# Kernel optimization log

Hardware: AMD Instinct MI355X
Metric: run time of the kernel (lower is better)

Reference implementation:

```python
import jax, jax.numpy as jnp
import numpy as np

V_DIM, Q_DIM, NUM_HID = 2048, 1024, 1024
B, K, N = 64, 12, 36


def setup_inputs() -> dict:
    key = jax.random.key(0)
    ks = jax.random.split(key, 8)
    v = jax.random.normal(ks[0], (B, K, N, V_DIM), dtype=jnp.float32)
    q = jax.random.normal(ks[1], (B, K, Q_DIM), dtype=jnp.float32)
    # FCNet layer: weight_norm(Linear(v_dim+q_dim, num_hid), dim=None) + ReLU
    W1 = jax.random.normal(ks[2], (NUM_HID, V_DIM + Q_DIM), dtype=jnp.float32) * 0.02
    g1 = jnp.asarray(1.0, dtype=jnp.float32)  # weight_norm gain (scalar, dim=None)
    b1 = jnp.zeros((NUM_HID,), dtype=jnp.float32)
    # final: weight_norm(Linear(num_hid, 1), dim=None)
    W2 = jax.random.normal(ks[3], (1, NUM_HID), dtype=jnp.float32) * 0.02
    g2 = jnp.asarray(1.0, dtype=jnp.float32)
    b2 = jnp.zeros((1,), dtype=jnp.float32)
    return {"v": v, "q": q, "W1": W1, "g1": g1, "b1": b1, "W2": W2, "g2": g2, "b2": b2}


def reference(v, q, W1, g1, b1, W2, g2, b2):
    # weight_norm with dim=None: W_eff = g * W / ||W||_F (g is a scalar)
    W1e = g1 * W1 / jnp.linalg.norm(W1)   # [num_hid, v_dim+q_dim]
    W2e = g2 * W2 / jnp.linalg.norm(W2)   # [1, num_hid]
    # Avoid materializing the repeated+concatenated [B,K,N,v_dim+q_dim] tensor:
    # cat(v, broadcast(q)) @ W1e^T == v @ W1v^T + q @ W1q^T (q term broadcast over N)
    W1v = W1e[:, :V_DIM]                  # [num_hid, v_dim]
    W1q = W1e[:, V_DIM:]                  # [num_hid, q_dim]
    hv = jnp.einsum('bknv,hv->bknh', v, W1v)          # [B,K,N,num_hid]
    hq = jnp.einsum('bkq,hq->bkh', q, W1q)            # [B,K,num_hid]
    joint = jax.nn.relu(hv + hq[:, :, None, :] + b1)  # FCNet: weight-norm Linear + ReLU
    logits = jnp.einsum('bknh,oh->bkno', joint, W2e) + b2  # [B,K,N,1]
    w = jax.nn.softmax(logits, axis=1)                # softmax over k (dim 1)
    return w
```

## Files before the change

### kernel.cpp

```cpp
#include <hip/hip_runtime.h>

#define V_DIM   2048
#define Q_DIM   1024
#define NUM_HID 1024
#define BB 64
#define KK 12
#define NN 36
#define M_ROWS (BB*KK*NN)
#define BKROWS (BB*KK)

typedef unsigned short u16;
typedef __bf16 bf16x8  __attribute__((ext_vector_type(8)));
typedef u16    ushort8 __attribute__((ext_vector_type(8)));
typedef float  floatx4 __attribute__((ext_vector_type(4)));

__device__ __forceinline__ unsigned cvtpk(float lo, float hi) {
    unsigned r;
    asm("v_cvt_pk_bf16_f32 %0, %1, %2" : "=v"(r) : "v"(lo), "v"(hi));
    return r;
}

__device__ __forceinline__ void gload16(const u16* g, u16* l) {
    __builtin_amdgcn_global_load_lds((const __attribute__((address_space(1))) void*)g,
                                     (__attribute__((address_space(3))) void*)l, 16, 0, 0);
}

__global__ void convert_w1_kernel(const float* __restrict__ W1,
                                  u16* __restrict__ W1v, u16* __restrict__ W1q,
                                  const float* __restrict__ W2,
                                  const float* __restrict__ g1,
                                  const float* __restrict__ g2,
                                  float* __restrict__ wsf)
{
    int s = blockIdx.x * 256 + threadIdx.x;
    int h = s / 384, g = s % 384;
    const float4* p = (const float4*)(W1 + (size_t)h * (V_DIM + Q_DIM) + g * 8);
    float4 a = p[0], b = p[1];
    float ss = a.x*a.x + a.y*a.y + a.z*a.z + a.w*a.w
             + b.x*b.x + b.y*b.y + b.z*b.z + b.w*b.w;
    unsigned d0 = cvtpk(a.x, a.y), d1 = cvtpk(a.z, a.w);
    unsigned d2 = cvtpk(b.x, b.y), d3 = cvtpk(b.z, b.w);
    uint4 o = make_uint4(d0, d1, d2, d3);
    if (g < 256) *(uint4*)(W1v + (size_t)h * V_DIM + g * 8) = o;
    else         *(uint4*)(W1q + (size_t)h * Q_DIM + (g - 256) * 8) = o;
    #pragma unroll
    for (int off = 32; off > 0; off >>= 1) ss += __shfl_down(ss, off);
    __shared__ float red[4];
    __shared__ bool  last;
    if ((threadIdx.x & 63) == 0) red[threadIdx.x >> 6] = ss;
    __syncthreads();
    if (threadIdx.x == 0) {
        atomicAdd(wsf, red[0] + red[1] + red[2] + red[3]);
        __threadfence();
        unsigned t = atomicAdd((unsigned*)(wsf + 1), 1u);
        last = (t == gridDim.x - 1);
    }
    __syncthreads();
    if (last) {
        float4 w = ((const float4*)W2)[threadIdx.x];
        float s2 = w.x*w.x + w.y*w.y + w.z*w.z + w.w*w.w;
        #pragma unroll
        for (int off = 32; off > 0; off >>= 1) s2 += __shfl_down(s2, off);
        __shared__ float red2[4];
        if ((threadIdx.x & 63) == 0) red2[threadIdx.x >> 6] = s2;
        __syncthreads();
        if (threadIdx.x == 0) {
            float w2ss = red2[0] + red2[1] + red2[2] + red2[3];
            float w1ss = atomicAdd(wsf, 0.0f);
            wsf[2] = g1[0] / sqrtf(w1ss);
            wsf[3] = g2[0] / sqrtf(w2ss);
        }
    }
}

template<int GK, bool MAIN>
__global__ __launch_bounds__(256, 2)
void gemm_kernel(const float* __restrict__ Asrc,
                 const u16*   __restrict__ Bsrc,
                 float*       __restrict__ outp,
                 const float* __restrict__ hq,
                 const float* __restrict__ b1,
                 const float* __restrict__ W2,
                 const float* __restrict__ scl)
{
    __shared__ u16 As[128 * 64];
    __shared__ u16 Bs[128 * 64];

    const int tid  = threadIdx.x;
    const int lane = tid & 63;
    const int wv   = tid >> 6;
    const int wm   = wv & 1;
    const int wn   = wv >> 1;
    const int quad = lane >> 4;
    const int l15  = lane & 15;

    const int bid  = blockIdx.y * 8 + blockIdx.x;
    const int nwg  = gridDim.x * gridDim.y;
    const int tile = (bid & 7) * (nwg >> 3) + (bid >> 3);
    const int tx   = tile & 7;
    const int ty   = tile >> 3;
    const int m0   = ty * 128;
    const int n0   = tx * 128;

    floatx4 acc[4][4];
    #pragma unroll
    for (int i = 0; i < 4; i++)
        #pragma unroll
        for (int j = 0; j < 4; j++)
            acc[i][j] = (floatx4){0.f, 0.f, 0.f, 0.f};

    for (int kt = 0; kt < GK / 64; ++kt) {
        const int k0 = kt * 64;
        __syncthreads();
        #pragma unroll
        for (int it = 0; it < 4; ++it) {
            int s = tid + 256 * it;
            int r = s >> 3, g = s & 7;
            const float4* gp = (const float4*)(Asrc + (size_t)(m0 + r) * GK + k0 + g * 8);
            float4 f0 = gp[0];
            float4 f1 = gp[1];
            unsigned d0 = cvtpk(f0.x, f0.y), d1 = cvtpk(f0.z, f0.w);
            unsigned d2 = cvtpk(f1.x, f1.y), d3 = cvtpk(f1.z, f1.w);
            *(uint4*)(&As[r * 64 + ((g ^ (r & 7)) * 8)]) = make_uint4(d0, d1, d2, d3);
        }
        #pragma unroll
        for (int it = 0; it < 4; ++it) {
            int sbase = it * 256 + wv * 64;
            int s = sbase + lane;
            int c = s >> 3, g = s & 7;
            int gs = g ^ (c & 7);
            gload16(Bsrc + (size_t)(n0 + c) * GK + k0 + gs * 8, &Bs[sbase * 8]);
        }
        __syncthreads();
        #pragma unroll
        for (int ks = 0; ks < 2; ++ks) {
            bf16x8 af[4], bfr[4];
            #pragma unroll
            for (int i = 0; i < 4; i++) {
                int rA = wm * 64 + i * 16 + l15;
                int offA = (ks * 32 + quad * 8) ^ ((rA & 7) << 3);
                af[i] = *(const bf16x8*)(&As[rA * 64 + offA]);
            }
            #pragma unroll
            for (int j = 0; j < 4; j++) {
                int c = wn * 64 + j * 16 + l15;
                int offB = (ks * 32 + quad * 8) ^ ((c & 7) << 3);
                bfr[j] = *(const bf16x8*)(&Bs[c * 64 + offB]);
            }
            #pragma unroll
            for (int i = 0; i < 4; i++)
                #pragma unroll
                for (int j = 0; j < 4; j++)
                    acc[i][j] = __builtin_amdgcn_mfma_f32_16x16x32_bf16(af[i], bfr[j], acc[i][j], 0, 0, 0);
        }
    }

    if constexpr (MAIN) {
        const float s1 = scl[2];
        int   cg[4];
        float w2v[4], b1v[4];
        #pragma unroll
        for (int j = 0; j < 4; j++) {
            cg[j]  = n0 + wn * 64 + j * 16 + l15;
            w2v[j] = W2[cg[j]];
            b1v[j] = b1[cg[j]];
        }
        #pragma unroll
        for (int i = 0; i < 4; i++) {
            #pragma unroll
            for (int r = 0; r < 4; r++) {
                const int mg = m0 + wm * 64 + i * 16 + quad * 4 + r;
                const int bk = mg / NN;
                float p = 0.f;
                #pragma unroll
                for (int j = 0; j < 4; j++) {
                    float pre = s1 * (acc[i][j][r] + hq[(size_t)bk * NUM_HID + cg[j]]) + b1v[j];
                    p += fmaxf(pre, 0.f) * w2v[j];
                }
                p += __shfl_xor(p, 1);
                p += __shfl_xor(p, 2);
                p += __shfl_xor(p, 4);
                p += __shfl_xor(p, 8);
                if (l15 == 0)
                    outp[(size_t)mg * 16 + tx * 2 + wn] = p;
            }
        }
    } else {
        #pragma unroll
        for (int i = 0; i < 4; i++)
            #pragma unroll
            for (int r = 0; r < 4; r++) {
                const int mg = m0 + wm * 64 + i * 16 + quad * 4 + r;
                #pragma unroll
                for (int j = 0; j < 4; j++) {
                    const int c = n0 + wn * 64 + j * 16 + l15;
                    outp[(size_t)mg * NUM_HID + c] = acc[i][j][r];
                }
            }
    }
}

__global__ void softmax_kernel(const float* __restrict__ part,
                               const float* __restrict__ scl,
                               const float* __restrict__ b2,
                               float* __restrict__ out)
{
    int t = blockIdx.x * 64 + threadIdx.x;
    int b = t / NN, n = t % NN;
    float s2 = scl[3], bias = b2[0];
    float lg[KK];
    float mx = -1e30f;
    #pragma unroll
    for (int k = 0; k < KK; k++) {
        int m = (b * KK + k) * NN + n;
        const float4* pp = (const float4*)(part + (size_t)m * 16);
        float4 a0 = pp[0], a1 = pp[1], a2 = pp[2], a3 = pp[3];
        float s = (a0.x + a0.y + a0.z + a0.w) + (a1.x + a1.y + a1.z + a1.w)
                + (a2.x + a2.y + a2.z + a2.w) + (a3.x + a3.y + a3.z + a3.w);
        lg[k] = s2 * s + bias;
        mx = fmaxf(mx, lg[k]);
    }
    float den = 0.f;
    #pragma unroll
    for (int k = 0; k < KK; k++) { lg[k] = expf(lg[k] - mx); den += lg[k]; }
    float inv = 1.0f / den;
    #pragma unroll
    for (int k = 0; k < KK; k++) out[(size_t)((b * KK + k) * NN + n)] = lg[k] * inv;
}

extern "C" void kernel_launch(void* const* d_in, const int* in_sizes, int n_in,
                              void* d_out, int out_size, void* d_ws, size_t ws_size,
                              hipStream_t stream)
{
    (void)in_sizes; (void)n_in; (void)out_size; (void)ws_size;
    const float* v  = (const float*)d_in[0];
    const float* q  = (const float*)d_in[1];
    const float* W1 = (const float*)d_in[2];
    const float* g1 = (const float*)d_in[3];
    const float* b1 = (const float*)d_in[4];
    const float* W2 = (const float*)d_in[5];
    const float* g2 = (const float*)d_in[6];
    const float* b2 = (const float*)d_in[7];
    float* out = (float*)d_out;

    char*  ws   = (char*)d_ws;
    float* wsf  = (float*)ws;
    float* hq   = (float*)(ws + 16);
    u16*   W1v  = (u16*)  (ws + 16 + 3145728);
    u16*   W1q  = (u16*)  (ws + 16 + 3145728 + 4194304);
    float* part = (float*)(ws + 16 + 3145728 + 4194304 + 2097152);

    hipMemsetAsync(d_ws, 0, 16, stream);
    convert_w1_kernel<<<1536, 256, 0, stream>>>(W1, W1v, W1q, W2, g1, g2, wsf);
    gemm_kernel<Q_DIM, false><<<dim3(8, 6), 256, 0, stream>>>(
        q, W1q, hq, nullptr, nullptr, nullptr, wsf);
    gemm_kernel<V_DIM, true><<<dim3(8, 216), 256, 0, stream>>>(
        v, W1v, part, hq, b1, W2, wsf);
    softmax_kernel<<<36, 64, 0, stream>>>(part, wsf, b2, out);
}
```

Baseline: 545.2 us.

## Double-buffer LDS tiles and prefetch A registers two stages ahead in GEMM

Replaces the single-buffered K-loop with a ping-pong LDS scheme. The B tile for the next step is loaded straight to LDS, and the fp32 A tile is prefetched into registers two iterations ahead, then converted to bf16 and written into the alternate buffer while the current tile feeds MFMAs. Manual vmcnt/lgkmcnt waits and a single barrier per iteration replace the two syncthreads. This aims to hide global load latency behind compute, at the cost of doubled LDS (64KB per block), which may reduce occupancy, plus extra prefetch registers.

```diff
diff --git a/kernel.cpp b/kernel.cpp
--- a/kernel.cpp
+++ b/kernel.cpp
@@ -83,8 +83,8 @@
                  const float* __restrict__ W2,
                  const float* __restrict__ scl)
 {
-    __shared__ u16 As[128 * 64];
-    __shared__ u16 Bs[128 * 64];
+    __shared__ u16 As[2][128 * 64];
+    __shared__ u16 Bs[2][128 * 64];
 
     const int tid  = threadIdx.x;
     const int lane = tid & 63;
@@ -93,6 +93,8 @@
     const int wn   = wv >> 1;
     const int quad = lane >> 4;
     const int l15  = lane & 15;
+    const int rr   = tid >> 3;
+    const int gcol = tid & 7;
 
     const int bid  = blockIdx.y * 8 + blockIdx.x;
     const int nwg  = gridDim.x * gridDim.y;
@@ -102,6 +104,8 @@
     const int m0   = ty * 128;
     const int n0   = tx * 128;
 
+    const int NT = GK / 64;
+
     floatx4 acc[4][4];
     #pragma unroll
     for (int i = 0; i < 4; i++)
@@ -109,51 +113,113 @@
         for (int j = 0; j < 4; j++)
             acc[i][j] = (floatx4){0.f, 0.f, 0.f, 0.f};
 
-    for (int kt = 0; kt < GK / 64; ++kt) {
-        const int k0 = kt * 64;
-        __syncthreads();
-        #pragma unroll
-        for (int it = 0; it < 4; ++it) {
-            int s = tid + 256 * it;
-            int r = s >> 3, g = s & 7;
-            const float4* gp = (const float4*)(Asrc + (size_t)(m0 + r) * GK + k0 + g * 8);
-            float4 f0 = gp[0];
-            float4 f1 = gp[1];
-            unsigned d0 = cvtpk(f0.x, f0.y), d1 = cvtpk(f0.z, f0.w);
-            unsigned d2 = cvtpk(f1.x, f1.y), d3 = cvtpk(f1.z, f1.w);
-            *(uint4*)(&As[r * 64 + ((g ^ (r & 7)) * 8)]) = make_uint4(d0, d1, d2, d3);
-        }
-        #pragma unroll
-        for (int it = 0; it < 4; ++it) {
-            int sbase = it * 256 + wv * 64;
-            int s = sbase + lane;
-            int c = s >> 3, g = s & 7;
-            int gs = g ^ (c & 7);
-            gload16(Bsrc + (size_t)(n0 + c) * GK + k0 + gs * 8, &Bs[sbase * 8]);
-        }
-        __syncthreads();
-        #pragma unroll
-        for (int ks = 0; ks < 2; ++ks) {
-            bf16x8 af[4], bfr[4];
-            #pragma unroll
-            for (int i = 0; i < 4; i++) {
-                int rA = wm * 64 + i * 16 + l15;
-                int offA = (ks * 32 + quad * 8) ^ ((rA & 7) << 3);
-                af[i] = *(const bf16x8*)(&As[rA * 64 + offA]);
-            }
-            #pragma unroll
-            for (int j = 0; j < 4; j++) {
-                int c = wn * 64 + j * 16 + l15;
-                int offB = (ks * 32 + quad * 8) ^ ((c & 7) << 3);
-                bfr[j] = *(const bf16x8*)(&Bs[c * 64 + offB]);
-            }
-            #pragma unroll
-            for (int i = 0; i < 4; i++)
-                #pragma unroll
-                for (int j = 0; j < 4; j++)
-                    acc[i][j] = __builtin_amdgcn_mfma_f32_16x16x32_bf16(af[i], bfr[j], acc[i][j], 0, 0, 0);
-        }
-    }
+    float4 pf0[8], pf1[8];
+
+#define ISSUE_A(t_, r_)                                                        \
+    {                                                                          \
+        _Pragma("unroll")                                                      \
+        for (int it = 0; it < 4; ++it) {                                       \
+            const float4* gp = (const float4*)(Asrc +                          \
+                (size_t)(m0 + rr + 32 * it) * GK + (t_) * 64 + gcol * 8);      \
+            r_[2 * it]     = gp[0];                                            \
+            r_[2 * it + 1] = gp[1];                                            \
+        }                                                                      \
+    }
+
+#define ISSUE_B(pn_, t_)                                                       \
+    {                                                                          \
+        _Pragma("unroll")                                                      \
+        for (int it = 0; it < 4; ++it) {                                       \
+            int sbase = it * 256 + wv * 64;                                    \
+            int s = sbase + lane;                                              \
+            int c = s >> 3, gg = s & 7;                                        \
+            int gs = gg ^ (c & 7);                                             \
+            gload16(Bsrc + (size_t)(n0 + c) * GK + (t_) * 64 + gs * 8,         \
+                    &Bs[pn_][sbase * 8]);                                      \
+        }                                                                      \
+    }
+
+#define CVT_WRITE(r_, pn_)                                                     \
+    {                                                                          \
+        _Pragma("unroll")                                                      \
+        for (int it = 0; it < 4; ++it) {                                       \
+            int row = rr + 32 * it;                                            \
+            unsigned d0 = cvtpk(r_[2*it].x,   r_[2*it].y);                     \
+            unsigned d1 = cvtpk(r_[2*it].z,   r_[2*it].w);                     \
+            unsigned d2 = cvtpk(r_[2*it+1].x, r_[2*it+1].y);                   \
+            unsigned d3 = cvtpk(r_[2*it+1].z, r_[2*it+1].w);                   \
+            *(uint4*)(&As[pn_][row * 64 + ((gcol ^ (row & 7)) * 8)]) =         \
+                make_uint4(d0, d1, d2, d3);                                    \
+        }                                                                      \
+    }
+
+#define COMPUTE(p_)                                                            \
+    {                                                                          \
+        _Pragma("unroll")                                                      \
+        for (int ks = 0; ks < 2; ++ks) {                                       \
+            bf16x8 af[4], bfr[4];                                              \
+            _Pragma("unroll")                                                  \
+            for (int i = 0; i < 4; i++) {                                      \
+                int ra_ = wm * 64 + i * 16 + l15;                              \
+                int offA = (ks * 32 + quad * 8) ^ ((ra_ & 7) << 3);            \
+                af[i] = *(const bf16x8*)(&As[p_][ra_ * 64 + offA]);            \
+            }                                                                  \
+            _Pragma("unroll")                                                  \
+            for (int j = 0; j < 4; j++) {                                      \
+                int c = wn * 64 + j * 16 + l15;                                \
+                int offB = (ks * 32 + quad * 8) ^ ((c & 7) << 3);              \
+                bfr[j] = *(const bf16x8*)(&Bs[p_][c * 64 + offB]);             \
+            }                                                                  \
+            _Pragma("unroll")                                                  \
+            for (int i = 0; i < 4; i++)                                        \
+                _Pragma("unroll")                                              \
+                for (int j = 0; j < 4; j++)                                    \
+                    acc[i][j] = __builtin_amdgcn_mfma_f32_16x16x32_bf16(       \
+                        af[i], bfr[j], acc[i][j], 0, 0, 0);                    \
+        }                                                                      \
+    }
+
+#define BODY(kt_, cur_, nxt_)                                                  \
+    {                                                                          \
+        const int p_  = (kt_) & 1;                                             \
+        const int pn_ = p_ ^ 1;                                                \
+        const int t1_ = ((kt_) + 1 < NT) ? (kt_) + 1 : NT - 1;                 \
+        const int t2_ = ((kt_) + 2 < NT) ? (kt_) + 2 : NT - 1;                 \
+        ISSUE_B(pn_, t1_);                                                     \
+        __builtin_amdgcn_sched_barrier(0);                                     \
+        ISSUE_A(t2_, nxt_);                                                    \
+        asm volatile("s_waitcnt vmcnt(12)" ::: "memory");                      \
+        CVT_WRITE(cur_, pn_);                                                  \
+        COMPUTE(p_);                                                           \
+        asm volatile("s_waitcnt vmcnt(8)" ::: "memory");                       \
+        asm volatile("s_waitcnt lgkmcnt(0)" ::: "memory");                     \
+        __builtin_amdgcn_s_barrier();                                          \
+        asm volatile("" ::: "memory");                                         \
+    }
+
+    ISSUE_A(0, pf0);
+    __builtin_amdgcn_sched_barrier(0);
+    ISSUE_B(0, 0);
+    __builtin_amdgcn_sched_barrier(0);
+    ISSUE_A(1, pf1);
+    asm volatile("s_waitcnt vmcnt(12)" ::: "memory");
+    CVT_WRITE(pf0, 0);
+    asm volatile("s_waitcnt vmcnt(8)" ::: "memory");
+    asm volatile("s_waitcnt lgkmcnt(0)" ::: "memory");
+    __builtin_amdgcn_s_barrier();
+    asm volatile("" ::: "memory");
+
+    for (int kt = 0; kt < NT; kt += 2) {
+        BODY(kt,     pf1, pf0);
+        BODY(kt + 1, pf0, pf1);
+    }
+    asm volatile("s_waitcnt vmcnt(0)" ::: "memory");
+
+#undef ISSUE_A
+#undef ISSUE_B
+#undef CVT_WRITE
+#undef COMPUTE
+#undef BODY
 
     if constexpr (MAIN) {
         const float s1 = scl[2];
```

Result: slower. 559.7 us (+2.6%).
